# Kernel optimization log

Hardware: AMD Instinct MI355X
Metric: run time of the kernel (lower is better)

## Reference

```python
import jax, jax.numpy as jnp
import numpy as np

N, E = 50000, 800000
HID, HEADS, EDIM = 64, 4, 32
HC = HID * HEADS
NEG_SLOPE = 0.2
LN_EPS = 1e-5


def setup_inputs() -> dict:
    key = jax.random.key(0)
    ks = jax.random.split(key, 16)
    s = lambda d: 1.0 / np.sqrt(d)
    return {
        "x": jax.random.normal(ks[0], (N, HID), jnp.float32),
        "edge_index": jax.random.randint(ks[1], (2, E), 0, N, jnp.int64),
        "edge_attr": jax.random.normal(ks[2], (E, EDIM), jnp.float32),
        # GATv2Conv params
        "W_l": jax.random.normal(ks[3], (HID, HC), jnp.float32) * s(HID),
        "b_l": jnp.zeros((HC,), jnp.float32),
        "W_r": jax.random.normal(ks[4], (HID, HC), jnp.float32) * s(HID),
        "b_r": jnp.zeros((HC,), jnp.float32),
        "W_e": jax.random.normal(ks[5], (EDIM, HC), jnp.float32) * s(EDIM),
        "att": jax.random.normal(ks[6], (HEADS, HID), jnp.float32) * s(HID),
        "bias_gat": jnp.zeros((HC,), jnp.float32),
        # block params
        "W1": jax.random.normal(ks[7], (HID, HC), jnp.float32) * s(HID),
        "b1": jnp.zeros((HC,), jnp.float32),
        "gamma": jnp.ones((HC,), jnp.float32),
        "beta": jnp.zeros((HC,), jnp.float32),
        "W2": jax.random.normal(ks[8], (HC, HID), jnp.float32) * s(HC),
        "b2": jnp.zeros((HID,), jnp.float32),
    }


def _gatv2(x, edge_index, edge_attr, W_l, b_l, W_r, b_r, W_e, att, bias_gat):
    src, dst = edge_index[0], edge_index[1]
    x_l = (x @ W_l + b_l).reshape(N, HEADS, HID)  # source transform
    x_r = (x @ W_r + b_r).reshape(N, HEADS, HID)  # target transform
    e = (edge_attr @ W_e).reshape(E, HEADS, HID)
    m = x_l[src] + x_r[dst] + e                    # [E, H, C]
    m = jax.nn.leaky_relu(m, NEG_SLOPE)
    alpha = jnp.einsum('ehc,hc->eh', m, att)       # [E, H]
    # segment softmax over incoming edges of each target node
    amax = jax.ops.segment_max(alpha, dst, num_segments=N)
    alpha = jnp.exp(alpha - amax[dst])
    denom = jax.ops.segment_sum(alpha, dst, num_segments=N)
    alpha = alpha / (denom[dst] + 1e-16)
    out = jax.ops.segment_sum(x_l[src] * alpha[..., None], dst, num_segments=N)
    return out.reshape(N, HC) + bias_gat


def reference(x, edge_index, edge_attr, W_l, b_l, W_r, b_r, W_e, att, bias_gat,
              W1, b1, gamma, beta, W2, b2):
    h = _gatv2(x, edge_index, edge_attr, W_l, b_l, W_r, b_r, W_e, att, bias_gat)
    xl = jnp.tanh(x @ W1 + b1)
    z = xl + h
    mu = jnp.mean(z, axis=-1, keepdims=True)
    var = jnp.var(z, axis=-1, keepdims=True)
    z = (z - mu) * jax.lax.rsqrt(var + LN_EPS) * gamma + beta
    return jnp.tanh(z @ W2 + b2)
```

## Files before the change

### kernel.cpp

```cpp
#include <hip/hip_runtime.h>
#include <math.h>

#define N_NODES 50000
#define N_EDGES 800000
#define HID 64
#define HEADS 4
#define HC 256
#define NEG_SLOPE 0.2f
#define LN_EPS 1e-5f
#define EDGE_BLOCKS 2048

typedef __attribute__((ext_vector_type(8))) short bf16x8;
typedef __attribute__((ext_vector_type(8))) unsigned short u16x8;
typedef __attribute__((ext_vector_type(4))) float f32x4;

__device__ __forceinline__ float bf2f(unsigned short u) {
    return __uint_as_float(((unsigned int)u) << 16);
}
__device__ __forceinline__ unsigned short f2bf(float f) {
    unsigned int u = __float_as_uint(f);
    u = (u + 0x7fffu + ((u >> 16) & 1u)) >> 16;
    return (unsigned short)u;
}
__device__ __forceinline__ float fast_tanh(float v) {
    const float c = fminf(fmaxf(v, -15.f), 15.f);
    const float e = __expf(2.f * c);
    return 1.f - 2.f / (e + 1.f);
}
__device__ __forceinline__ bf16x8 pack_bf8(float4 a, float4 b) {
    u16x8 r;
    r[0] = f2bf(a.x); r[1] = f2bf(a.y); r[2] = f2bf(a.z); r[3] = f2bf(a.w);
    r[4] = f2bf(b.x); r[5] = f2bf(b.y); r[6] = f2bf(b.z); r[7] = f2bf(b.w);
    return __builtin_bit_cast(bf16x8, r);
}

__global__ __launch_bounds__(256) void k_node_transform(
    const float* __restrict__ x,
    const float* __restrict__ W_l, const float* __restrict__ b_l,
    const float* __restrict__ W_r, const float* __restrict__ b_r,
    unsigned short* __restrict__ xl_t, unsigned short* __restrict__ xr_t)
{
    __shared__ float xs[16][64];
    __shared__ unsigned short tl[16][256], tr[16][256];
    const int n0 = blockIdx.x * 16;
    const int t = threadIdx.x;
    for (int i = t; i < 16 * 64; i += 256) xs[i >> 6][i & 63] = x[n0 * 64 + i];
    __syncthreads();

    float accl[16], accr[16];
    const float bl = b_l[t], br = b_r[t];
#pragma unroll
    for (int n = 0; n < 16; n++) { accl[n] = bl; accr[n] = br; }
    for (int k = 0; k < 64; k++) {
        const float wl = W_l[k * 256 + t];
        const float wr = W_r[k * 256 + t];
#pragma unroll
        for (int n = 0; n < 16; n++) {
            accl[n] = fmaf(xs[n][k], wl, accl[n]);
            accr[n] = fmaf(xs[n][k], wr, accr[n]);
        }
    }
    const int pos = (t & 15) * 16 + (t >> 4);
#pragma unroll
    for (int n = 0; n < 16; n++) {
        tl[n][pos] = f2bf(accl[n]);
        tr[n][pos] = f2bf(accr[n]);
    }
    __syncthreads();
    const int n = t >> 4, q = t & 15;
#pragma unroll
    for (int i = 0; i < 4; i++) {
        *(ushort4*)(xl_t + (size_t)(n0 + n) * 256 + q * 16 + i * 4) = *(const ushort4*)&tl[n][q * 16 + i * 4];
        *(ushort4*)(xr_t + (size_t)(n0 + n) * 256 + q * 16 + i * 4) = *(const ushort4*)&tr[n][q * 16 + i * 4];
    }
}

__global__ __launch_bounds__(256) void k_hist(const int* __restrict__ ei, int* __restrict__ count)
{
    const int e = blockIdx.x * 256 + threadIdx.x;
    if (e < N_EDGES) atomicAdd(&count[ei[N_EDGES + e]], 1);
}

__global__ __launch_bounds__(1024) void k_scan(const int* __restrict__ count, int* __restrict__ off)
{
    __shared__ int wsum[16];
    __shared__ int s_carry;
    const int t = threadIdx.x, lane = t & 63, wv = t >> 6;
    if (t == 0) s_carry = 0;
    __syncthreads();
    for (int base = 0; base < N_NODES; base += 8192) {
        const int idx0 = base + t * 8;
        int v[8];
#pragma unroll
        for (int j = 0; j < 8; j++) { int i = idx0 + j; v[j] = (i < N_NODES) ? count[i] : 0; }
#pragma unroll
        for (int j = 1; j < 8; j++) v[j] += v[j - 1];
        const int tot = v[7];
        int sc = tot;
#pragma unroll
        for (int s = 1; s < 64; s <<= 1) { int o = __shfl_up(sc, s, 64); if (lane >= s) sc += o; }
        if (lane == 63) wsum[wv] = sc;
        __syncthreads();
        const int carry = s_carry;
        int woff = 0;
        for (int u = 0; u < wv; u++) woff += wsum[u];
        const int ebase = carry + woff + (sc - tot);
#pragma unroll
        for (int j = 0; j < 8; j++) {
            int i = idx0 + j;
            if (i < N_NODES) off[i] = ebase + (j ? v[j - 1] : 0);
        }
        __syncthreads();
        if (t == 0) { int tt = 0; for (int u = 0; u < 16; u++) tt += wsum[u]; s_carry = carry + tt; }
        __syncthreads();
    }
    if (threadIdx.x == 0) off[N_NODES] = s_carry;
}

__global__ __launch_bounds__(256) void k_scatter(
    const int* __restrict__ ei, const int* __restrict__ off, int* __restrict__ cursor,
    int* __restrict__ csr_src, int* __restrict__ eid_csr)
{
    const int e = blockIdx.x * 256 + threadIdx.x;
    if (e < N_EDGES) {
        const int s = ei[e];
        const int d = ei[N_EDGES + e];
        const int pos = off[d] + atomicAdd(&cursor[d], 1);
        csr_src[pos] = s;
        eid_csr[pos] = e;
    }
}

template<bool F32>
__global__ __launch_bounds__(256) void k_edgeagg(
    const int* __restrict__ off, const int* __restrict__ csr_src,
    const int* __restrict__ eid_csr, const float* __restrict__ edge_attr,
    const float* __restrict__ W_e, const float* __restrict__ att,
    const unsigned short* __restrict__ xl_t, const unsigned short* __restrict__ xr_t,
    void* __restrict__ zs_g)
{
    __shared__ unsigned short bfrag_s[16][64][8];

    const int t = threadIdx.x;
    const int lane = t & 63, wv = t >> 6;
    const int arow = lane & 15, koct = lane >> 4;

    for (int i = t; i < 1024; i += 256) {
        const int nt = i >> 6, ls = i & 63;
        const int col = nt * 16 + (ls & 15);
        const int kb = (ls >> 4) * 8;
        unsigned short tmp[8];
#pragma unroll
        for (int j = 0; j < 8; j++) tmp[j] = f2bf(W_e[(kb + j) * 256 + col]);
        *(ushort4*)&bfrag_s[nt][ls][0] = make_ushort4(tmp[0], tmp[1], tmp[2], tmp[3]);
        *(ushort4*)&bfrag_s[nt][ls][4] = make_ushort4(tmp[4], tmp[5], tmp[6], tmp[7]);
    }
    __syncthreads();

    float attLf[8], attHf[8];
#pragma unroll
    for (int j = 0; j < 8; j++) {
        attLf[j] = att[j * 16 + arow];
        attHf[j] = att[(j + 8) * 16 + arow];
    }

    const int STRIDE = EDGE_BLOCKS * 4;
    int node = blockIdx.x * 4 + wv;
    if (node >= N_NODES) return;

    int lo = off[node], hi = off[node + 1];
    u16x8 xrl = *(const u16x8*)(xr_t + (size_t)node * 256 + arow * 16);
    u16x8 xrh = *(const u16x8*)(xr_t + (size_t)node * 256 + arow * 16 + 8);
    while (hi <= lo) {
#pragma unroll
        for (int q = 0; q < 4; q++) {
            const int nt = koct * 4 + q;
            if (F32) ((float*)zs_g)[(size_t)node * 256 + nt * 16 + arow] = 0.f;
            else ((unsigned short*)zs_g)[(size_t)node * 256 + nt * 16 + arow] = 0;
        }
        node += STRIDE;
        if (node >= N_NODES) return;
        lo = off[node]; hi = off[node + 1];
        xrl = *(const u16x8*)(xr_t + (size_t)node * 256 + arow * 16);
        xrh = *(const u16x8*)(xr_t + (size_t)node * 256 + arow * 16 + 8);
    }
    int svbase = lo;
    int svall = csr_src[min(svbase + lane, hi - 1)];
    int evall = eid_csr[min(svbase + lane, hi - 1)];

    int nnode = node + STRIDE;
    bool nvalid = nnode < N_NODES;
    int nlo = 0, nhi = 0, nsvall = 0, nevall = 0;
    u16x8 nxrl = xrl, nxrh = xrh;
    if (nvalid) {
        nlo = off[nnode]; nhi = off[nnode + 1];
        nxrl = *(const u16x8*)(xr_t + (size_t)nnode * 256 + arow * 16);
        nxrh = *(const u16x8*)(xr_t + (size_t)nnode * 256 + arow * 16 + 8);
        if (nhi > nlo) {
            nsvall = csr_src[min(nlo + lane, nhi - 1)];
            nevall = eid_csr[min(nlo + lane, nhi - 1)];
        }
    }
    int p0 = lo;
    bf16x8 af;
    u16x8 xlo[4], xhi[4];
    {
        const int eid0 = __shfl(evall, arow, 64);
        const float* ap = edge_attr + (size_t)eid0 * 32 + koct * 8;
        af = pack_bf8(*(const float4*)ap, *(const float4*)(ap + 4));
#pragma unroll
        for (int r = 0; r < 4; r++) {
            const int sr = __shfl(svall, koct * 4 + r, 64);
            const unsigned short* bp = xl_t + (size_t)sr * 256 + arow * 16;
            xlo[r] = *(const u16x8*)bp;
            xhi[r] = *(const u16x8*)(bp + 8);
        }
    }

    float g[16];
#pragma unroll
    for (int i = 0; i < 16; i++) g[i] = 0.f;
    float dsum[4] = {0.f, 0.f, 0.f, 0.f};

    for (;;) {
        const bool last = (p0 + 16 >= hi);
        bool uvalid;
        int up0;
        if (!last) { uvalid = true; up0 = p0 + 16; }
        else {
            while (nvalid && nlo >= nhi) {
#pragma unroll
                for (int q = 0; q < 4; q++) {
                    const int nt = koct * 4 + q;
                    if (F32) ((float*)zs_g)[(size_t)nnode * 256 + nt * 16 + arow] = 0.f;
                    else ((unsigned short*)zs_g)[(size_t)nnode * 256 + nt * 16 + arow] = 0;
                }
                nnode += STRIDE;
                nvalid = nnode < N_NODES;
                if (nvalid) {
                    nlo = off[nnode]; nhi = off[nnode + 1];
                    nxrl = *(const u16x8*)(xr_t + (size_t)nnode * 256 + arow * 16);
                    nxrh = *(const u16x8*)(xr_t + (size_t)nnode * 256 + arow * 16 + 8);
                    if (nhi > nlo) {
                        nsvall = csr_src[min(nlo + lane, nhi - 1)];
                        nevall = eid_csr[min(nlo + lane, nhi - 1)];
                    }
                }
            }
            uvalid = nvalid; up0 = nlo;
        }
        float4 uA0 = make_float4(0.f, 0.f, 0.f, 0.f), uA1 = uA0;
        if (uvalid) {
            const int ubase = last ? 0 : (up0 - svbase);
            const int uev = last ? nevall : evall;
            const int ueid = __shfl(uev, ubase + arow, 64);
            const float* ap = edge_attr + (size_t)ueid * 32 + koct * 8;
            uA0 = *(const float4*)ap;
            uA1 = *(const float4*)(ap + 4);
        }

        float s_[4][4];
#pragma unroll
        for (int r = 0; r < 4; r++)
#pragma unroll
            for (int h = 0; h < 4; h++) s_[r][h] = 0.f;

#pragma unroll
        for (int nt = 0; nt < 8; nt++) {
            const bf16x8 bfr = *(const bf16x8*)&bfrag_s[nt][lane][0];
            const float xrv = bf2f((unsigned short)xrl[nt]);
            f32x4 dacc = {xrv, xrv, xrv, xrv};
            dacc = __builtin_amdgcn_mfma_f32_16x16x32_bf16(af, bfr, dacc, 0, 0, 0);
            const float atv = attLf[nt];
            const int h = nt >> 2;
#pragma unroll
            for (int r = 0; r < 4; r++) {
                const float mm = dacc[r] + bf2f((unsigned short)xlo[r][nt]);
                const float lk = fmaxf(mm, NEG_SLOPE * mm);
                s_[r][h] = fmaf(atv, lk, s_[r][h]);
            }
        }
        u16x8 uxlo[4], uxhi[4];
        if (uvalid) {
            const int ubase = last ? 0 : (up0 - svbase);
            const int usrcv = last ? nsvall : svall;
#pragma unroll
            for (int r = 0; r < 4; r++) {
                const int sr = __shfl(usrcv, ubase + koct * 4 + r, 64);
                const unsigned short* bp = xl_t + (size_t)sr * 256 + arow * 16;
                uxlo[r] = *(const u16x8*)bp;
                uxhi[r] = *(const u16x8*)(bp + 8);
            }
        } else {
#pragma unroll
            for (int r = 0; r < 4; r++) { uxlo[r] = xlo[r]; uxhi[r] = xhi[r]; }
        }
#pragma unroll
        for (int n2 = 0; n2 < 8; n2++) {
            const int nt = n2 + 8;
            const bf16x8 bfr = *(const bf16x8*)&bfrag_s[nt][lane][0];
            const float xrv = bf2f((unsigned short)xrh[n2]);
            f32x4 dacc = {xrv, xrv, xrv, xrv};
            dacc = __builtin_amdgcn_mfma_f32_16x16x32_bf16(af, bfr, dacc, 0, 0, 0);
            const float atv = attHf[n2];
            const int h = nt >> 2;
#pragma unroll
            for (int r = 0; r < 4; r++) {
                const float mm = dacc[r] + bf2f((unsigned short)xhi[r][n2]);
                const float lk = fmaxf(mm, NEG_SLOPE * mm);
                s_[r][h] = fmaf(atv, lk, s_[r][h]);
            }
        }
#pragma unroll
        for (int r = 0; r < 4; r++)
#pragma unroll
            for (int h = 0; h < 4; h++) {
                float v = s_[r][h];
                v += __shfl_xor(v, 1, 64);
                v += __shfl_xor(v, 2, 64);
                v += __shfl_xor(v, 4, 64);
                v += __shfl_xor(v, 8, 64);
                s_[r][h] = v;
            }
#pragma unroll
        for (int h = 0; h < 4; h++) {
            float w4[4];
#pragma unroll
            for (int r = 0; r < 4; r++) {
                const bool ok = (p0 + koct * 4 + r) < hi;
                w4[r] = ok ? __expf(fminf(s_[r][h], 60.f)) : 0.f;
            }
            dsum[h] += (w4[0] + w4[1]) + (w4[2] + w4[3]);
#pragma unroll
            for (int q = 0; q < 4; q++) {
                const int nt = h * 4 + q;
                float acc = g[nt];
#pragma unroll
                for (int r = 0; r < 4; r++) {
                    const float xv = bf2f((unsigned short)(nt < 8 ? xlo[r][nt & 7] : xhi[r][nt & 7]));
                    acc = fmaf(w4[r], xv, acc);
                }
                g[nt] = acc;
            }
        }

        if (last) {
#pragma unroll
            for (int i = 0; i < 16; i++) {
                float v = g[i];
                v += __shfl_xor(v, 16, 64);
                v += __shfl_xor(v, 32, 64);
                g[i] = v;
            }
#pragma unroll
            for (int h = 0; h < 4; h++) {
                float v = dsum[h];
                v += __shfl_xor(v, 16, 64);
                v += __shfl_xor(v, 32, 64);
                dsum[h] = v;
            }
            float inv[4];
#pragma unroll
            for (int h = 0; h < 4; h++) inv[h] = 1.f / (dsum[h] + 1e-16f);
#pragma unroll
            for (int q = 0; q < 4; q++) {
                const int nt = koct * 4 + q;
                const float v = g[nt] * inv[nt >> 2];
                if (F32) ((float*)zs_g)[(size_t)node * 256 + nt * 16 + arow] = v;
                else ((unsigned short*)zs_g)[(size_t)node * 256 + nt * 16 + arow] = f2bf(v);
            }
            if (!uvalid) return;
            node = nnode; lo = nlo; hi = nhi; xrl = nxrl; xrh = nxrh;
            svbase = nlo; svall = nsvall; evall = nevall;
#pragma unroll
            for (int i = 0; i < 16; i++) g[i] = 0.f;
#pragma unroll
            for (int h = 0; h < 4; h++) dsum[h] = 0.f;
            nnode += STRIDE;
            nvalid = nnode < N_NODES;
            if (nvalid) {
                nlo = off[nnode]; nhi = off[nnode + 1];
                nxrl = *(const u16x8*)(xr_t + (size_t)nnode * 256 + arow * 16);
                nxrh = *(const u16x8*)(xr_t + (size_t)nnode * 256 + arow * 16 + 8);
                if (nhi > nlo) {
                    nsvall = csr_src[min(nlo + lane, nhi - 1)];
                    nevall = eid_csr[min(nlo + lane, nhi - 1)];
                }
            }
        }
        p0 = up0;
        af = pack_bf8(uA0, uA1);
#pragma unroll
        for (int r = 0; r < 4; r++) { xlo[r] = uxlo[r]; xhi[r] = uxhi[r]; }
        if (p0 - svbase >= 32) {
            svbase = p0;
            svall = csr_src[min(svbase + lane, hi - 1)];
            evall = eid_csr[min(svbase + lane, hi - 1)];
        }
    }
}

template<bool F32>
__global__ __launch_bounds__(256) void k_post(
    const void* __restrict__ zs_g, const float* __restrict__ x,
    const float* __restrict__ bias_gat,
    const float* __restrict__ W1, const float* __restrict__ b1,
    const float* __restrict__ gamma, const float* __restrict__ beta,
    const float* __restrict__ W2, const float* __restrict__ b2,
    float* __restrict__ out)
{
    __shared__ float xs[16][64];
    __shared__ float zsh[16][256];
    __shared__ float part[16][4][64];
    __shared__ float redS[16][4], redQ[16][4];

    const int n0 = blockIdx.x * 16;
    const int t = threadIdx.x, lane = t & 63, wv = t >> 6;

    for (int i = t; i < 16 * 64; i += 256) xs[i >> 6][i & 63] = x[n0 * 64 + i];
    __syncthreads();

    float a1[16];
    const float b1v = b1[t];
#pragma unroll
    for (int n = 0; n < 16; n++) a1[n] = b1v;
    for (int k = 0; k < 64; k++) {
        const float w1v = W1[k * 256 + t];
#pragma unroll
        for (int n = 0; n < 16; n++) a1[n] = fmaf(xs[n][k], w1v, a1[n]);
    }

    const float bg = bias_gat[t];
    float z[16];
#pragma unroll
    for (int n = 0; n < 16; n++) {
        const float gv = F32 ? ((const float*)zs_g)[(size_t)(n0 + n) * 256 + t]
                             : bf2f(((const unsigned short*)zs_g)[(size_t)(n0 + n) * 256 + t]);
        z[n] = fast_tanh(a1[n]) + gv + bg;
    }

    const float gm = gamma[t], bt = beta[t];
#pragma unroll
    for (int n = 0; n < 16; n++) {
        float s = z[n], q = z[n] * z[n];
#pragma unroll
        for (int m = 1; m < 64; m <<= 1) { s += __shfl_xor(s, m, 64); q += __shfl_xor(q, m, 64); }
        if (lane == 0) { redS[n][wv] = s; redQ[n][wv] = q; }
    }
    __syncthreads();
#pragma unroll
    for (int n = 0; n < 16; n++) {
        const float s = redS[n][0] + redS[n][1] + redS[n][2] + redS[n][3];
        const float q = redQ[n][0] + redQ[n][1] + redQ[n][2] + redQ[n][3];
        const float mu = s * (1.f / 256.f);
        const float var = q * (1.f / 256.f) - mu * mu;
        const float ivn = rsqrtf(var + LN_EPS);
        zsh[n][t] = (z[n] - mu) * ivn * gm + bt;
    }
    __syncthreads();

    const int j = t & 63, qq = t >> 6;
    float p[16];
#pragma unroll
    for (int n = 0; n < 16; n++) p[n] = 0.f;
    for (int c0 = 0; c0 < 64; c0++) {
        const int c = qq * 64 + c0;
        const float w2v = W2[c * 64 + j];
#pragma unroll
        for (int n = 0; n < 16; n++) p[n] = fmaf(zsh[n][c], w2v, p[n]);
    }
#pragma unroll
    for (int n = 0; n < 16; n++) part[n][qq][j] = p[n];
    __syncthreads();
#pragma unroll
    for (int i = 0; i < 4; i++) {
        const int n = wv * 4 + i;
        const float s = part[n][0][lane] + part[n][1][lane] + part[n][2][lane] + part[n][3][lane];
        out[(size_t)(n0 + n) * 64 + lane] = fast_tanh(s + b2[lane]);
    }
}

extern "C" void kernel_launch(void* const* d_in, const int* in_sizes, int n_in,
                              void* d_out, int out_size, void* d_ws, size_t ws_size,
                              hipStream_t stream)
{
    const float* x         = (const float*)d_in[0];
    const int*   ei        = (const int*)d_in[1];
    const float* edge_attr = (const float*)d_in[2];
    const float* W_l       = (const float*)d_in[3];
    const float* b_l       = (const float*)d_in[4];
    const float* W_r       = (const float*)d_in[5];
    const float* b_r       = (const float*)d_in[6];
    const float* W_e       = (const float*)d_in[7];
    const float* att       = (const float*)d_in[8];
    const float* bias_gat  = (const float*)d_in[9];
    const float* W1        = (const float*)d_in[10];
    const float* b1        = (const float*)d_in[11];
    const float* gamma     = (const float*)d_in[12];
    const float* beta      = (const float*)d_in[13];
    const float* W2        = (const float*)d_in[14];
    const float* b2        = (const float*)d_in[15];
    float* out = (float*)d_out;

    char* wsb = (char*)d_ws;
    size_t o = 0;
    unsigned short* xl_t   = (unsigned short*)(wsb + o);  o += (size_t)N_NODES * HC * 2;
    unsigned short* xr_t   = (unsigned short*)(wsb + o);  o += (size_t)N_NODES * HC * 2;
    int* csr_src           = (int*)(wsb + o);             o += (size_t)N_EDGES * 4;
    int* eid_csr           = (int*)(wsb + o);             o += (size_t)N_EDGES * 4;
    int* count             = (int*)(wsb + o);             o += (size_t)N_NODES * 4;
    int* cursor            = (int*)(wsb + o);             o += (size_t)N_NODES * 4;
    int* off               = (int*)(wsb + o);             o += (size_t)(N_NODES + 1) * 4;
    o = (o + 255) & ~(size_t)255;
    void* zs_g             = (void*)(wsb + o);
    const bool f32ok = (o + (size_t)N_NODES * HC * 4) <= ws_size;

    hipMemsetAsync(count, 0, 2 * (size_t)N_NODES * sizeof(int), stream);

    k_node_transform<<<N_NODES / 16, 256, 0, stream>>>(x, W_l, b_l, W_r, b_r, xl_t, xr_t);
    k_hist<<<(N_EDGES + 255) / 256, 256, 0, stream>>>(ei, count);
    k_scan<<<1, 1024, 0, stream>>>(count, off);
    k_scatter<<<(N_EDGES + 255) / 256, 256, 0, stream>>>(ei, off, cursor, csr_src, eid_csr);
    if (f32ok) {
        k_edgeagg<true><<<EDGE_BLOCKS, 256, 0, stream>>>(off, csr_src, eid_csr, edge_attr,
                                                         W_e, att, xl_t, xr_t, zs_g);
        k_post<true><<<N_NODES / 16, 256, 0, stream>>>(zs_g, x, bias_gat,
                                                       W1, b1, gamma, beta, W2, b2, out);
    } else {
        k_edgeagg<false><<<EDGE_BLOCKS, 256, 0, stream>>>(off, csr_src, eid_csr, edge_attr,
                                                          W_e, att, xl_t, xr_t, zs_g);
        k_post<false><<<N_NODES / 16, 256, 0, stream>>>(zs_g, x, bias_gat,
                                                        W1, b1, gamma, beta, W2, b2, out);
    }
}
```

Baseline: 590.0 us.

## Use MFMA for node transform and permute channel layout to vectorize aggregation stores

Replaces the scalar FMA node-transform kernel with a bf16 MFMA version that stages W_l/W_r in shared memory in fragment order and writes the MFMA output layout directly. The channel order of the aggregated output changes so each lane writes a contiguous float4 or ushort4 instead of four strided scalars. A small kernel permutes W1, W2, b1, gamma, beta and bias_gat so the post kernel matches this new channel order. This adds an extra launch and more bf16 rounding of weights, and it depends on the permutation being consistent everywhere.

```diff
diff --git a/kernel.cpp b/kernel.cpp
--- a/kernel.cpp
+++ b/kernel.cpp
@@ -34,45 +34,98 @@
     return __builtin_bit_cast(bf16x8, r);
 }
 
-__global__ __launch_bounds__(256) void k_node_transform(
+__global__ __launch_bounds__(256) void k_ntm(
     const float* __restrict__ x,
     const float* __restrict__ W_l, const float* __restrict__ b_l,
     const float* __restrict__ W_r, const float* __restrict__ b_r,
     unsigned short* __restrict__ xl_t, unsigned short* __restrict__ xr_t)
 {
-    __shared__ float xs[16][64];
-    __shared__ unsigned short tl[16][256], tr[16][256];
-    const int n0 = blockIdx.x * 16;
-    const int t = threadIdx.x;
-    for (int i = t; i < 16 * 64; i += 256) xs[i >> 6][i & 63] = x[n0 * 64 + i];
-    __syncthreads();
-
-    float accl[16], accr[16];
-    const float bl = b_l[t], br = b_r[t];
-#pragma unroll
-    for (int n = 0; n < 16; n++) { accl[n] = bl; accr[n] = br; }
-    for (int k = 0; k < 64; k++) {
-        const float wl = W_l[k * 256 + t];
-        const float wr = W_r[k * 256 + t];
-#pragma unroll
-        for (int n = 0; n < 16; n++) {
-            accl[n] = fmaf(xs[n][k], wl, accl[n]);
-            accr[n] = fmaf(xs[n][k], wr, accr[n]);
-        }
-    }
-    const int pos = (t & 15) * 16 + (t >> 4);
-#pragma unroll
-    for (int n = 0; n < 16; n++) {
-        tl[n][pos] = f2bf(accl[n]);
-        tr[n][pos] = f2bf(accr[n]);
-    }
-    __syncthreads();
-    const int n = t >> 4, q = t & 15;
-#pragma unroll
-    for (int i = 0; i < 4; i++) {
-        *(ushort4*)(xl_t + (size_t)(n0 + n) * 256 + q * 16 + i * 4) = *(const ushort4*)&tl[n][q * 16 + i * 4];
-        *(ushort4*)(xr_t + (size_t)(n0 + n) * 256 + q * 16 + i * 4) = *(const ushort4*)&tr[n][q * 16 + i * 4];
-    }
+    __shared__ unsigned short wl_s[2][16][64][8];
+    __shared__ unsigned short wr_s[2][16][64][8];
+    const int t = threadIdx.x, lane = t & 63, wv = t >> 6;
+    const int arow = lane & 15, koct = lane >> 4;
+
+    for (int i = t; i < 2048; i += 256) {
+        const int ks = i >> 10, nt = (i >> 6) & 15, ls = i & 63;
+        const int col = nt * 16 + (ls & 15);
+        const int kb = ks * 32 + (ls >> 4) * 8;
+        unsigned short a[8], b[8];
+#pragma unroll
+        for (int j = 0; j < 8; j++) {
+            a[j] = f2bf(W_l[(kb + j) * 256 + col]);
+            b[j] = f2bf(W_r[(kb + j) * 256 + col]);
+        }
+        *(ushort4*)&wl_s[ks][nt][ls][0] = make_ushort4(a[0], a[1], a[2], a[3]);
+        *(ushort4*)&wl_s[ks][nt][ls][4] = make_ushort4(a[4], a[5], a[6], a[7]);
+        *(ushort4*)&wr_s[ks][nt][ls][0] = make_ushort4(b[0], b[1], b[2], b[3]);
+        *(ushort4*)&wr_s[ks][nt][ls][4] = make_ushort4(b[4], b[5], b[6], b[7]);
+    }
+    __syncthreads();
+
+    const int n0w = blockIdx.x * 64 + wv * 16;
+    if (n0w >= N_NODES) return;
+
+    const float* xrow = x + (size_t)(n0w + arow) * 64;
+    const bf16x8 af0 = pack_bf8(*(const float4*)(xrow + koct * 8),
+                                *(const float4*)(xrow + koct * 8 + 4));
+    const bf16x8 af1 = pack_bf8(*(const float4*)(xrow + 32 + koct * 8),
+                                *(const float4*)(xrow + 32 + koct * 8 + 4));
+
+    float acc[4][16];
+#pragma unroll
+    for (int nt = 0; nt < 16; nt++) {
+        const float bv = b_l[nt * 16 + arow];
+        f32x4 d = {bv, bv, bv, bv};
+        d = __builtin_amdgcn_mfma_f32_16x16x32_bf16(af0, *(const bf16x8*)&wl_s[0][nt][lane][0], d, 0, 0, 0);
+        d = __builtin_amdgcn_mfma_f32_16x16x32_bf16(af1, *(const bf16x8*)&wl_s[1][nt][lane][0], d, 0, 0, 0);
+#pragma unroll
+        for (int r = 0; r < 4; r++) acc[r][nt] = d[r];
+    }
+#pragma unroll
+    for (int r = 0; r < 4; r++) {
+        u16x8 lo, hi;
+#pragma unroll
+        for (int j = 0; j < 8; j++) { lo[j] = f2bf(acc[r][j]); hi[j] = f2bf(acc[r][j + 8]); }
+        unsigned short* dst = xl_t + (size_t)(n0w + koct * 4 + r) * 256 + arow * 16;
+        *(u16x8*)dst = lo;
+        *(u16x8*)(dst + 8) = hi;
+    }
+#pragma unroll
+    for (int nt = 0; nt < 16; nt++) {
+        const float bv = b_r[nt * 16 + arow];
+        f32x4 d = {bv, bv, bv, bv};
+        d = __builtin_amdgcn_mfma_f32_16x16x32_bf16(af0, *(const bf16x8*)&wr_s[0][nt][lane][0], d, 0, 0, 0);
+        d = __builtin_amdgcn_mfma_f32_16x16x32_bf16(af1, *(const bf16x8*)&wr_s[1][nt][lane][0], d, 0, 0, 0);
+#pragma unroll
+        for (int r = 0; r < 4; r++) acc[r][nt] = d[r];
+    }
+#pragma unroll
+    for (int r = 0; r < 4; r++) {
+        u16x8 lo, hi;
+#pragma unroll
+        for (int j = 0; j < 8; j++) { lo[j] = f2bf(acc[r][j]); hi[j] = f2bf(acc[r][j + 8]); }
+        unsigned short* dst = xr_t + (size_t)(n0w + koct * 4 + r) * 256 + arow * 16;
+        *(u16x8*)dst = lo;
+        *(u16x8*)(dst + 8) = hi;
+    }
+}
+
+__global__ __launch_bounds__(256) void k_permw(
+    const float* __restrict__ W1, const float* __restrict__ b1,
+    const float* __restrict__ gamma, const float* __restrict__ beta,
+    const float* __restrict__ bias_gat, const float* __restrict__ W2,
+    float* __restrict__ W1p, float* __restrict__ b1p,
+    float* __restrict__ gammap, float* __restrict__ betap,
+    float* __restrict__ biasgp, float* __restrict__ W2p)
+{
+    const int c = threadIdx.x;
+    const int pos = (c & 15) * 16 + (c >> 4);
+    for (int k = 0; k < 64; k++) W1p[k * 256 + pos] = W1[k * 256 + c];
+    b1p[pos] = b1[c];
+    gammap[pos] = gamma[c];
+    betap[pos] = beta[c];
+    biasgp[pos] = bias_gat[c];
+    for (int j = 0; j < 64; j++) W2p[pos * 64 + j] = W2[c * 64 + j];
 }
 
 __global__ __launch_bounds__(256) void k_hist(const int* __restrict__ ei, int* __restrict__ count)
@@ -172,12 +225,8 @@
     u16x8 xrl = *(const u16x8*)(xr_t + (size_t)node * 256 + arow * 16);
     u16x8 xrh = *(const u16x8*)(xr_t + (size_t)node * 256 + arow * 16 + 8);
     while (hi <= lo) {
-#pragma unroll
-        for (int q = 0; q < 4; q++) {
-            const int nt = koct * 4 + q;
-            if (F32) ((float*)zs_g)[(size_t)node * 256 + nt * 16 + arow] = 0.f;
-            else ((unsigned short*)zs_g)[(size_t)node * 256 + nt * 16 + arow] = 0;
-        }
+        if (F32) *(float4*)((float*)zs_g + (size_t)node * 256 + arow * 16 + koct * 4) = make_float4(0.f, 0.f, 0.f, 0.f);
+        else *(ushort4*)((unsigned short*)zs_g + (size_t)node * 256 + arow * 16 + koct * 4) = make_ushort4(0, 0, 0, 0);
         node += STRIDE;
         if (node >= N_NODES) return;
         lo = off[node]; hi = off[node + 1];
@@ -229,12 +278,8 @@
         if (!last) { uvalid = true; up0 = p0 + 16; }
         else {
             while (nvalid && nlo >= nhi) {
-#pragma unroll
-                for (int q = 0; q < 4; q++) {
-                    const int nt = koct * 4 + q;
-                    if (F32) ((float*)zs_g)[(size_t)nnode * 256 + nt * 16 + arow] = 0.f;
-                    else ((unsigned short*)zs_g)[(size_t)nnode * 256 + nt * 16 + arow] = 0;
-                }
+                if (F32) *(float4*)((float*)zs_g + (size_t)nnode * 256 + arow * 16 + koct * 4) = make_float4(0.f, 0.f, 0.f, 0.f);
+                else *(ushort4*)((unsigned short*)zs_g + (size_t)nnode * 256 + arow * 16 + koct * 4) = make_ushort4(0, 0, 0, 0);
                 nnode += STRIDE;
                 nvalid = nnode < N_NODES;
                 if (nvalid) {
@@ -359,15 +404,15 @@
                 v += __shfl_xor(v, 32, 64);
                 dsum[h] = v;
             }
-            float inv[4];
-#pragma unroll
-            for (int h = 0; h < 4; h++) inv[h] = 1.f / (dsum[h] + 1e-16f);
-#pragma unroll
-            for (int q = 0; q < 4; q++) {
-                const int nt = koct * 4 + q;
-                const float v = g[nt] * inv[nt >> 2];
-                if (F32) ((float*)zs_g)[(size_t)node * 256 + nt * 16 + arow] = v;
-                else ((unsigned short*)zs_g)[(size_t)node * 256 + nt * 16 + arow] = f2bf(v);
+            const float inv = 1.f / (dsum[koct] + 1e-16f);
+            if (F32) {
+                *(float4*)((float*)zs_g + (size_t)node * 256 + arow * 16 + koct * 4) =
+                    make_float4(g[koct * 4] * inv, g[koct * 4 + 1] * inv,
+                                g[koct * 4 + 2] * inv, g[koct * 4 + 3] * inv);
+            } else {
+                *(ushort4*)((unsigned short*)zs_g + (size_t)node * 256 + arow * 16 + koct * 4) =
+                    make_ushort4(f2bf(g[koct * 4] * inv), f2bf(g[koct * 4 + 1] * inv),
+                                 f2bf(g[koct * 4 + 2] * inv), f2bf(g[koct * 4 + 3] * inv));
             }
             if (!uvalid) return;
             node = nnode; lo = nlo; hi = nhi; xrl = nxrl; xrh = nxrh;
@@ -403,10 +448,10 @@
 template<bool F32>
 __global__ __launch_bounds__(256) void k_post(
     const void* __restrict__ zs_g, const float* __restrict__ x,
-    const float* __restrict__ bias_gat,
-    const float* __restrict__ W1, const float* __restrict__ b1,
-    const float* __restrict__ gamma, const float* __restrict__ beta,
-    const float* __restrict__ W2, const float* __restrict__ b2,
+    const float* __restrict__ biasgp,
+    const float* __restrict__ W1p, const float* __restrict__ b1p,
+    const float* __restrict__ gammap, const float* __restrict__ betap,
+    const float* __restrict__ W2p, const float* __restrict__ b2,
     float* __restrict__ out)
 {
     __shared__ float xs[16][64];
@@ -421,16 +466,16 @@
     __syncthreads();
 
     float a1[16];
-    const float b1v = b1[t];
+    const float b1v = b1p[t];
 #pragma unroll
     for (int n = 0; n < 16; n++) a1[n] = b1v;
     for (int k = 0; k < 64; k++) {
-        const float w1v = W1[k * 256 + t];
+        const float w1v = W1p[k * 256 + t];
 #pragma unroll
         for (int n = 0; n < 16; n++) a1[n] = fmaf(xs[n][k], w1v, a1[n]);
     }
 
-    const float bg = bias_gat[t];
+    const float bg = biasgp[t];
     float z[16];
 #pragma unroll
     for (int n = 0; n < 16; n++) {
@@ -439,7 +484,7 @@
         z[n] = fast_tanh(a1[n]) + gv + bg;
     }
 
-    const float gm = gamma[t], bt = beta[t];
+    const float gm = gammap[t], bt = betap[t];
 #pragma unroll
     for (int n = 0; n < 16; n++) {
         float s = z[n], q = z[n] * z[n];
@@ -465,7 +510,7 @@
     for (int n = 0; n < 16; n++) p[n] = 0.f;
     for (int c0 = 0; c0 < 64; c0++) {
         const int c = qq * 64 + c0;
-        const float w2v = W2[c * 64 + j];
+        const float w2v = W2p[c * 64 + j];
 #pragma unroll
         for (int n = 0; n < 16; n++) p[n] = fmaf(zsh[n][c], w2v, p[n]);
     }
@@ -511,25 +556,33 @@
     int* count             = (int*)(wsb + o);             o += (size_t)N_NODES * 4;
     int* cursor            = (int*)(wsb + o);             o += (size_t)N_NODES * 4;
     int* off               = (int*)(wsb + o);             o += (size_t)(N_NODES + 1) * 4;
+    float* W1p             = (float*)(wsb + o);           o += 64 * 256 * 4;
+    float* W2p             = (float*)(wsb + o);           o += 256 * 64 * 4;
+    float* b1p             = (float*)(wsb + o);           o += 256 * 4;
+    float* gammap          = (float*)(wsb + o);           o += 256 * 4;
+    float* betap           = (float*)(wsb + o);           o += 256 * 4;
+    float* biasgp          = (float*)(wsb + o);           o += 256 * 4;
     o = (o + 255) & ~(size_t)255;
     void* zs_g             = (void*)(wsb + o);
     const bool f32ok = (o + (size_t)N_NODES * HC * 4) <= ws_size;
 
     hipMemsetAsync(count, 0, 2 * (size_t)N_NODES * sizeof(int), stream);
 
-    k_node_transform<<<N_NODES / 16, 256, 0, stream>>>(x, W_l, b_l, W_r, b_r, xl_t, xr_t);
+    k_ntm<<<(N_NODES + 63) / 64, 256, 0, stream>>>(x, W_l, b_l, W_r, b_r, xl_t, xr_t);
+    k_permw<<<1, 256, 0, stream>>>(W1, b1, gamma, beta, bias_gat, W2,
+                                   W1p, b1p, gammap, betap, biasgp, W2p);
     k_hist<<<(N_EDGES + 255) / 256, 256, 0, stream>>>(ei, count);
     k_scan<<<1, 1024, 0, stream>>>(count, off);
     k_scatter<<<(N_EDGES + 255) / 256, 256, 0, stream>>>(ei, off, cursor, csr_src, eid_csr);
     if (f32ok) {
         k_edgeagg<true><<<EDGE_BLOCKS, 256, 0, stream>>>(off, csr_src, eid_csr, edge_attr,
                                                          W_e, att, xl_t, xr_t, zs_g);
-        k_post<true><<<N_NODES / 16, 256, 0, stream>>>(zs_g, x, bias_gat,
-                                                       W1, b1, gamma, beta, W2, b2, out);
+        k_post<true><<<N_NODES / 16, 256, 0, stream>>>(zs_g, x, biasgp,
+                                                       W1p, b1p, gammap, betap, W2p, b2, out);
     } else {
         k_edgeagg<false><<<EDGE_BLOCKS, 256, 0, stream>>>(off, csr_src, eid_csr, edge_attr,
                                                           W_e, att, xl_t, xr_t, zs_g);
-        k_post<false><<<N_NODES / 16, 256, 0, stream>>>(zs_g, x, bias_gat,
-                                                        W1, b1, gamma, beta, W2, b2, out);
-    }
-}
+        k_post<false><<<N_NODES / 16, 256, 0, stream>>>(zs_g, x, biasgp,
+                                                        W1p, b1p, gammap, betap, W2p, b2, out);
+    }
+}
```

After: 560.8 us. 1.05x faster.
